# Kernel optimization log

Measured on AMD Instinct MI355X. Metric: run time of the kernel, lower is better.

## Reference

```python
import jax, jax.numpy as jnp
import numpy as np

M = 4096   # out_features
N = 4096   # in_features
K_NNZ = 204  # nnz per row -> keep_ratio ~ 0.05
T = 8192   # tokens (batch*seq)


def setup_inputs() -> dict:
    key = jax.random.key(0)
    k1, k2, k3, k4 = jax.random.split(key, 4)
    # CSR structure: K_NNZ unique sorted columns per row (constant index buffers)
    rng = np.random.default_rng(0)
    cols = np.argsort(rng.random((M, N)), axis=1)[:, :K_NNZ]
    cols = np.sort(cols, axis=1).astype(np.int32)
    col_idx = jnp.asarray(cols.reshape(-1))                      # [nnz]
    row_ids = jnp.asarray(np.repeat(np.arange(M, dtype=np.int32), K_NNZ))  # [nnz]
    x = jax.random.normal(k1, (T, N), dtype=jnp.float32)
    dense_weight = jax.random.normal(k2, (M, N), dtype=jnp.float32) * 0.02
    bias = jax.random.normal(k3, (M,), dtype=jnp.float32) * 0.02
    sparse_values = jax.random.normal(k4, (M * K_NNZ,), dtype=jnp.float32) * 0.02
    return {"x": x, "dense_weight": dense_weight, "bias": bias,
            "sparse_values": sparse_values, "row_ids": row_ids, "col_idx": col_idx}


def reference(x, dense_weight, bias, sparse_values, row_ids, col_idx):
    # sp_add: scatter CSR values into the frozen dense weight (W = W_dense + W_sparse)
    W = dense_weight.at[row_ids, col_idx].add(sparse_values)     # [M, N]
    # sp_mm hot path: y = x @ W^T + b
    return jnp.dot(x, W.T) + bias                                # [T, M]
```

## Files before the change

### kernel.cpp

```cpp
#include <hip/hip_runtime.h>


typedef __attribute__((ext_vector_type(8))) __bf16 bf16x8;
typedef __attribute__((ext_vector_type(4))) float f32x4;
typedef __attribute__((ext_vector_type(8))) unsigned short u16x8;

#define BARRIER()   asm volatile("s_barrier" ::: "memory")
#define WAITVM0()   asm volatile("s_waitcnt vmcnt(0)" ::: "memory")

__device__ __forceinline__ unsigned short f2bf(float f) {
  unsigned int u = __builtin_bit_cast(unsigned int, f);
  u += 0x7FFFu + ((u >> 16) & 1u);
  return (unsigned short)(u >> 16);
}

__global__ __launch_bounds__(256) void cvt_f32_bf16(
    const float* __restrict__ s, unsigned short* __restrict__ d, long n8) {
  long i = (long)blockIdx.x * blockDim.x + threadIdx.x;
  const long stride = (long)gridDim.x * blockDim.x;
  for (; i < n8; i += stride) {
    const float4* sp = (const float4*)(s + i * 8);
    float4 a = sp[0];
    float4 b = sp[1];
    u16x8 o;
    o[0] = f2bf(a.x); o[1] = f2bf(a.y); o[2] = f2bf(a.z); o[3] = f2bf(a.w);
    o[4] = f2bf(b.x); o[5] = f2bf(b.y); o[6] = f2bf(b.z); o[7] = f2bf(b.w);
    *(u16x8*)(d + i * 8) = o;
  }
}

__global__ __launch_bounds__(256) void sparse_scatter(
    const float* __restrict__ dense, const float* __restrict__ vals,
    const int* __restrict__ rows, const int* __restrict__ cols,
    unsigned short* __restrict__ Wb, int nnz, int K) {
  int i = blockIdx.x * blockDim.x + threadIdx.x;
  if (i < nnz) {
    size_t off = (size_t)rows[i] * (size_t)K + (size_t)cols[i];
    Wb[off] = f2bf(dense[off] + vals[i]);
  }
}

__global__ __launch_bounds__(512, 2) void gemm256p(
    const unsigned short* __restrict__ A,
    const unsigned short* __restrict__ B,
    const float* __restrict__ bias,
    float* __restrict__ C,
    int Tm, int Mn, int K) {
  extern __shared__ __align__(16) char smem[];

  const int tid  = threadIdx.x;
  const int lane = tid & 63;
  const int wid  = tid >> 6;
  const int wm = (wid >> 2) * 128;
  const int wn = (wid & 3) * 64;

  const int nwg = gridDim.x;
  int bid = blockIdx.x;
  if ((nwg & 7) == 0) bid = (bid & 7) * (nwg >> 3) + (bid >> 3);
  const int ntn = Mn >> 8;
  const int bm0 = (bid / ntn) << 8;
  const int bn0 = (bid % ntn) << 8;

  const int NT = K >> 6;

  const int sr  = tid >> 3;
  const int gq8 = ((tid & 7) ^ (sr & 7)) * 8;
  const unsigned short* Asrc = A + (size_t)(bm0 + sr) * K + gq8;
  const unsigned short* Bsrc = B + (size_t)(bn0 + sr) * K + gq8;
  const size_t r64 = (size_t)64 * K;
  const int ldst = tid * 16;

#define STAGEH(SRC, H, LDSB, KOFF) do {                                          \
    __builtin_amdgcn_global_load_lds(                                            \
      (const __attribute__((address_space(1))) void*)((SRC) + (size_t)(H)*2*r64 + (KOFF)), \
      (__attribute__((address_space(3))) void*)(smem + (LDSB) + ldst), 16, 0, 0);\
    __builtin_amdgcn_global_load_lds(                                            \
      (const __attribute__((address_space(1))) void*)((SRC) + (size_t)(H)*2*r64 + r64 + (KOFF)), \
      (__attribute__((address_space(3))) void*)(smem + (LDSB) + 8192 + ldst), 16, 0, 0); \
  } while (0)

  const int fr = lane & 15, cq = lane >> 4;
  const int f7 = fr & 7;
  const int q0 = ((cq ^ f7) << 4);
  const int q1 = (((4 + cq) ^ f7) << 4);
  const int arow = (wm + fr) * 128;
  const int brow = (wn + fr) * 128;

  f32x4 acc[8][4] = {};
  bf16x8 aq0[4], aq1[4], bA0[2], bA1[2], bB0[2], bB1[2];

  STAGEH(Asrc, 0, 0, 0);
  STAGEH(Asrc, 1, 16384, 0);
  STAGEH(Bsrc, 0, 32768, 0);
  STAGEH(Bsrc, 1, 49152, 0);
  WAITVM0();
  BARRIER();

#pragma unroll 2
  for (int t = 0; t < NT; ++t) {
    const char* Ab = smem + (t & 1) * 65536;
    const char* Bb = Ab + 32768;
    const int nbase = ((t & 1) ^ 1) * 65536;
    const int kn = (t + 1) * 64;
    const bool st = (t + 1 < NT);

#pragma unroll
    for (int m = 0; m < 4; ++m) {
      aq0[m] = *(const bf16x8*)(Ab + arow + m * 2048 + q0);
      aq1[m] = *(const bf16x8*)(Ab + arow + m * 2048 + q1);
    }
#pragma unroll
    for (int n = 0; n < 2; ++n) {
      bA0[n] = *(const bf16x8*)(Bb + brow + n * 2048 + q0);
      bA1[n] = *(const bf16x8*)(Bb + brow + n * 2048 + q1);
    }
    if (st) { STAGEH(Asrc, 0, nbase, kn); STAGEH(Asrc, 1, nbase + 16384, kn); }
    BARRIER();
    __builtin_amdgcn_s_setprio(1);
#pragma unroll
    for (int m = 0; m < 4; ++m)
#pragma unroll
      for (int n = 0; n < 2; ++n) {
        acc[m][n] = __builtin_amdgcn_mfma_f32_16x16x32_bf16(aq0[m], bA0[n], acc[m][n], 0, 0, 0);
        acc[m][n] = __builtin_amdgcn_mfma_f32_16x16x32_bf16(aq1[m], bA1[n], acc[m][n], 0, 0, 0);
      }
    __builtin_amdgcn_s_setprio(0);
    BARRIER();

#pragma unroll
    for (int n = 0; n < 2; ++n) {
      bB0[n] = *(const bf16x8*)(Bb + brow + (n + 2) * 2048 + q0);
      bB1[n] = *(const bf16x8*)(Bb + brow + (n + 2) * 2048 + q1);
    }
    if (st) { STAGEH(Bsrc, 0, nbase + 32768, kn); STAGEH(Bsrc, 1, nbase + 49152, kn); }
    BARRIER();
    __builtin_amdgcn_s_setprio(1);
#pragma unroll
    for (int m = 0; m < 4; ++m)
#pragma unroll
      for (int n = 0; n < 2; ++n) {
        acc[m][n + 2] = __builtin_amdgcn_mfma_f32_16x16x32_bf16(aq0[m], bB0[n], acc[m][n + 2], 0, 0, 0);
        acc[m][n + 2] = __builtin_amdgcn_mfma_f32_16x16x32_bf16(aq1[m], bB1[n], acc[m][n + 2], 0, 0, 0);
      }
    __builtin_amdgcn_s_setprio(0);
    BARRIER();

#pragma unroll
    for (int m = 0; m < 4; ++m) {
      aq0[m] = *(const bf16x8*)(Ab + arow + (m + 4) * 2048 + q0);
      aq1[m] = *(const bf16x8*)(Ab + arow + (m + 4) * 2048 + q1);
    }
    BARRIER();
    __builtin_amdgcn_s_setprio(1);
#pragma unroll
    for (int m = 0; m < 4; ++m)
#pragma unroll
      for (int n = 0; n < 2; ++n) {
        acc[m + 4][n] = __builtin_amdgcn_mfma_f32_16x16x32_bf16(aq0[m], bA0[n], acc[m + 4][n], 0, 0, 0);
        acc[m + 4][n] = __builtin_amdgcn_mfma_f32_16x16x32_bf16(aq1[m], bA1[n], acc[m + 4][n], 0, 0, 0);
      }
    __builtin_amdgcn_s_setprio(0);
    BARRIER();

    __builtin_amdgcn_s_setprio(1);
#pragma unroll
    for (int m = 0; m < 4; ++m)
#pragma unroll
      for (int n = 0; n < 2; ++n) {
        acc[m + 4][n + 2] = __builtin_amdgcn_mfma_f32_16x16x32_bf16(aq0[m], bB0[n], acc[m + 4][n + 2], 0, 0, 0);
        acc[m + 4][n + 2] = __builtin_amdgcn_mfma_f32_16x16x32_bf16(aq1[m], bB1[n], acc[m + 4][n + 2], 0, 0, 0);
      }
    __builtin_amdgcn_s_setprio(0);
    WAITVM0();
    BARRIER();
  }
#undef STAGEH

  const int c4 = cq * 4;
#pragma unroll
  for (int n = 0; n < 4; ++n) {
    const int col = bn0 + wn + n * 16 + fr;
    const float bv = bias[col];
#pragma unroll
    for (int m = 0; m < 8; ++m) {
      const size_t rowb = (size_t)(bm0 + wm + m * 16 + c4);
#pragma unroll
      for (int q = 0; q < 4; ++q)
        C[(rowb + q) * (size_t)Mn + col] = acc[m][n][q] + bv;
    }
  }
}

extern "C" void kernel_launch(void* const* d_in, const int* in_sizes, int n_in,
                              void* d_out, int out_size, void* d_ws, size_t ws_size,
                              hipStream_t stream) {
  const float* x     = (const float*)d_in[0];
  const float* dw    = (const float*)d_in[1];
  const float* bias  = (const float*)d_in[2];
  const float* sv    = (const float*)d_in[3];
  const int*   rows  = (const int*)d_in[4];
  const int*   cols  = (const int*)d_in[5];
  float* out = (float*)d_out;

  const int  Mn = in_sizes[2];
  const long wElems = (long)in_sizes[1];
  const int  K  = (int)(wElems / Mn);
  const long xElems = (long)in_sizes[0];
  const int  Tm = (int)(xElems / K);
  const int  nnz = in_sizes[3];

  unsigned short* Wb = (unsigned short*)d_ws;
  unsigned short* Xb = Wb + wElems;

  cvt_f32_bf16<<<2048, 256, 0, stream>>>(dw, Wb, wElems / 8);
  sparse_scatter<<<(nnz + 255) / 256, 256, 0, stream>>>(dw, sv, rows, cols, Wb, nnz, K);
  cvt_f32_bf16<<<2048, 256, 0, stream>>>(x, Xb, xElems / 8);

  dim3 grid((Tm >> 8) * (Mn >> 8));
  gemm256p<<<grid, 512, 131072, stream>>>(Xb, Wb, bias, out, Tm, Mn, K);
}
```

Baseline: 313.6 us.

## Restructure GEMM main loop into 8-phase ping-pong with staggered partial vmcnt waits

Unrolls the K loop by two with fixed even/odd LDS buffers and spreads the global-to-LDS stages across eight MFMA phases. B tiles are prefetched one step further ahead, so each iteration waits with vmcnt(4) instead of draining all outstanding loads. It also adds lgkmcnt waits and scheduling barriers before each MFMA quad. The goal is to overlap memory latency with compute. The trade-off is more complex buffer-hazard reasoning and some risk of races, since loads are issued into buffers still being read.

Measured after the change: 306.7 us. 1.02x faster.

```diff
diff --git a/kernel.cpp b/kernel.cpp
--- a/kernel.cpp
+++ b/kernel.cpp
@@ -6,7 +6,9 @@
 typedef __attribute__((ext_vector_type(8))) unsigned short u16x8;
 
 #define BARRIER()   asm volatile("s_barrier" ::: "memory")
-#define WAITVM0()   asm volatile("s_waitcnt vmcnt(0)" ::: "memory")
+#define WAITLGKM0() asm volatile("s_waitcnt lgkmcnt(0)" ::: "memory")
+#define WAITVM(n)   asm volatile("s_waitcnt vmcnt(" #n ")" ::: "memory")
+#define SCHED0()    __builtin_amdgcn_sched_barrier(0)
 
 __device__ __forceinline__ unsigned short f2bf(float f) {
   unsigned int u = __builtin_bit_cast(unsigned int, f);
@@ -40,7 +42,7 @@
   }
 }
 
-__global__ __launch_bounds__(512, 2) void gemm256p(
+__global__ __launch_bounds__(512, 2) void gemm8p(
     const unsigned short* __restrict__ A,
     const unsigned short* __restrict__ B,
     const float* __restrict__ bias,
@@ -93,87 +95,112 @@
   STAGEH(Asrc, 1, 16384, 0);
   STAGEH(Bsrc, 0, 32768, 0);
   STAGEH(Bsrc, 1, 49152, 0);
-  WAITVM0();
+  STAGEH(Bsrc, 0, 98304, 64);
+  STAGEH(Bsrc, 1, 114688, 64);
+  WAITVM(4);
   BARRIER();
 
-#pragma unroll 2
-  for (int t = 0; t < NT; ++t) {
-    const char* Ab = smem + (t & 1) * 65536;
-    const char* Bb = Ab + 32768;
-    const int nbase = ((t & 1) ^ 1) * 65536;
-    const int kn = (t + 1) * 64;
-    const bool st = (t + 1 < NT);
-
-#pragma unroll
-    for (int m = 0; m < 4; ++m) {
-      aq0[m] = *(const bf16x8*)(Ab + arow + m * 2048 + q0);
-      aq1[m] = *(const bf16x8*)(Ab + arow + m * 2048 + q1);
-    }
-#pragma unroll
-    for (int n = 0; n < 2; ++n) {
-      bA0[n] = *(const bf16x8*)(Bb + brow + n * 2048 + q0);
-      bA1[n] = *(const bf16x8*)(Bb + brow + n * 2048 + q1);
-    }
-    if (st) { STAGEH(Asrc, 0, nbase, kn); STAGEH(Asrc, 1, nbase + 16384, kn); }
-    BARRIER();
-    __builtin_amdgcn_s_setprio(1);
-#pragma unroll
-    for (int m = 0; m < 4; ++m)
-#pragma unroll
-      for (int n = 0; n < 2; ++n) {
-        acc[m][n] = __builtin_amdgcn_mfma_f32_16x16x32_bf16(aq0[m], bA0[n], acc[m][n], 0, 0, 0);
-        acc[m][n] = __builtin_amdgcn_mfma_f32_16x16x32_bf16(aq1[m], bA1[n], acc[m][n], 0, 0, 0);
-      }
-    __builtin_amdgcn_s_setprio(0);
-    BARRIER();
-
-#pragma unroll
-    for (int n = 0; n < 2; ++n) {
-      bB0[n] = *(const bf16x8*)(Bb + brow + (n + 2) * 2048 + q0);
-      bB1[n] = *(const bf16x8*)(Bb + brow + (n + 2) * 2048 + q1);
-    }
-    if (st) { STAGEH(Bsrc, 0, nbase + 32768, kn); STAGEH(Bsrc, 1, nbase + 49152, kn); }
-    BARRIER();
-    __builtin_amdgcn_s_setprio(1);
-#pragma unroll
-    for (int m = 0; m < 4; ++m)
-#pragma unroll
-      for (int n = 0; n < 2; ++n) {
-        acc[m][n + 2] = __builtin_amdgcn_mfma_f32_16x16x32_bf16(aq0[m], bB0[n], acc[m][n + 2], 0, 0, 0);
-        acc[m][n + 2] = __builtin_amdgcn_mfma_f32_16x16x32_bf16(aq1[m], bB1[n], acc[m][n + 2], 0, 0, 0);
-      }
-    __builtin_amdgcn_s_setprio(0);
-    BARRIER();
-
-#pragma unroll
-    for (int m = 0; m < 4; ++m) {
-      aq0[m] = *(const bf16x8*)(Ab + arow + (m + 4) * 2048 + q0);
-      aq1[m] = *(const bf16x8*)(Ab + arow + (m + 4) * 2048 + q1);
-    }
-    BARRIER();
-    __builtin_amdgcn_s_setprio(1);
-#pragma unroll
-    for (int m = 0; m < 4; ++m)
-#pragma unroll
-      for (int n = 0; n < 2; ++n) {
-        acc[m + 4][n] = __builtin_amdgcn_mfma_f32_16x16x32_bf16(aq0[m], bA0[n], acc[m + 4][n], 0, 0, 0);
-        acc[m + 4][n] = __builtin_amdgcn_mfma_f32_16x16x32_bf16(aq1[m], bA1[n], acc[m + 4][n], 0, 0, 0);
-      }
-    __builtin_amdgcn_s_setprio(0);
-    BARRIER();
-
-    __builtin_amdgcn_s_setprio(1);
-#pragma unroll
-    for (int m = 0; m < 4; ++m)
-#pragma unroll
-      for (int n = 0; n < 2; ++n) {
-        acc[m + 4][n + 2] = __builtin_amdgcn_mfma_f32_16x16x32_bf16(aq0[m], bB0[n], acc[m + 4][n + 2], 0, 0, 0);
-        acc[m + 4][n + 2] = __builtin_amdgcn_mfma_f32_16x16x32_bf16(aq1[m], bB1[n], acc[m + 4][n + 2], 0, 0, 0);
-      }
-    __builtin_amdgcn_s_setprio(0);
-    WAITVM0();
-    BARRIER();
-  }
+#define QUAD(MB, NB, AQ0, AQ1, BL0, BL1) do {                                    \
+    __builtin_amdgcn_s_setprio(1);                                               \
+    _Pragma("unroll")                                                            \
+    for (int m = 0; m < 4; ++m)                                                  \
+      _Pragma("unroll")                                                          \
+      for (int n = 0; n < 2; ++n) {                                              \
+        acc[m+(MB)][n+(NB)] = __builtin_amdgcn_mfma_f32_16x16x32_bf16(           \
+            AQ0[m], BL0[n], acc[m+(MB)][n+(NB)], 0, 0, 0);                       \
+        acc[m+(MB)][n+(NB)] = __builtin_amdgcn_mfma_f32_16x16x32_bf16(           \
+            AQ1[m], BL1[n], acc[m+(MB)][n+(NB)], 0, 0, 0);                       \
+      }                                                                          \
+    __builtin_amdgcn_s_setprio(0);                                               \
+  } while (0)
+
+  for (int j = 0; j < (NT >> 1); ++j) {
+    const int t2 = 2 * j + 2, t3 = 2 * j + 3;
+    const int k1 = (2 * j + 1) << 6, k2 = t2 << 6, k3 = t3 << 6;
+    const char* AbE = smem;            const char* BbE = smem + 32768;
+    const char* AbO = smem + 65536;    const char* BbO = smem + 98304;
+
+#pragma unroll
+    for (int m = 0; m < 4; ++m) {
+      aq0[m] = *(const bf16x8*)(AbE + arow + m * 2048 + q0);
+      aq1[m] = *(const bf16x8*)(AbE + arow + m * 2048 + q1);
+    }
+#pragma unroll
+    for (int n = 0; n < 2; ++n) {
+      bA0[n] = *(const bf16x8*)(BbE + brow + n * 2048 + q0);
+      bA1[n] = *(const bf16x8*)(BbE + brow + n * 2048 + q1);
+    }
+    STAGEH(Asrc, 0, 65536, k1);
+    BARRIER(); WAITLGKM0(); SCHED0();
+    QUAD(0, 0, aq0, aq1, bA0, bA1);
+    BARRIER();
+
+#pragma unroll
+    for (int n = 0; n < 2; ++n) {
+      bB0[n] = *(const bf16x8*)(BbE + brow + (n + 2) * 2048 + q0);
+      bB1[n] = *(const bf16x8*)(BbE + brow + (n + 2) * 2048 + q1);
+    }
+    STAGEH(Asrc, 1, 81920, k1);
+    BARRIER(); WAITLGKM0(); SCHED0();
+    QUAD(0, 2, aq0, aq1, bB0, bB1);
+    BARRIER();
+
+#pragma unroll
+    for (int m = 0; m < 4; ++m) {
+      aq0[m] = *(const bf16x8*)(AbE + arow + (m + 4) * 2048 + q0);
+      aq1[m] = *(const bf16x8*)(AbE + arow + (m + 4) * 2048 + q1);
+    }
+    if (t2 < NT) STAGEH(Bsrc, 0, 32768, k2);
+    BARRIER(); WAITLGKM0(); SCHED0();
+    QUAD(4, 0, aq0, aq1, bA0, bA1);
+    BARRIER();
+
+    if (t2 < NT) STAGEH(Bsrc, 1, 49152, k2);
+    QUAD(4, 2, aq0, aq1, bB0, bB1);
+    if (t2 < NT) { WAITVM(4); } else { WAITVM(0); }
+    BARRIER();
+
+#pragma unroll
+    for (int m = 0; m < 4; ++m) {
+      aq0[m] = *(const bf16x8*)(AbO + arow + m * 2048 + q0);
+      aq1[m] = *(const bf16x8*)(AbO + arow + m * 2048 + q1);
+    }
+#pragma unroll
+    for (int n = 0; n < 2; ++n) {
+      bA0[n] = *(const bf16x8*)(BbO + brow + n * 2048 + q0);
+      bA1[n] = *(const bf16x8*)(BbO + brow + n * 2048 + q1);
+    }
+    if (t2 < NT) STAGEH(Asrc, 0, 0, k2);
+    BARRIER(); WAITLGKM0(); SCHED0();
+    QUAD(0, 0, aq0, aq1, bA0, bA1);
+    BARRIER();
+
+#pragma unroll
+    for (int n = 0; n < 2; ++n) {
+      bB0[n] = *(const bf16x8*)(BbO + brow + (n + 2) * 2048 + q0);
+      bB1[n] = *(const bf16x8*)(BbO + brow + (n + 2) * 2048 + q1);
+    }
+    if (t2 < NT) STAGEH(Asrc, 1, 16384, k2);
+    BARRIER(); WAITLGKM0(); SCHED0();
+    QUAD(0, 2, aq0, aq1, bB0, bB1);
+    BARRIER();
+
+#pragma unroll
+    for (int m = 0; m < 4; ++m) {
+      aq0[m] = *(const bf16x8*)(AbO + arow + (m + 4) * 2048 + q0);
+      aq1[m] = *(const bf16x8*)(AbO + arow + (m + 4) * 2048 + q1);
+    }
+    if (t3 < NT) STAGEH(Bsrc, 0, 98304, k3);
+    BARRIER(); WAITLGKM0(); SCHED0();
+    QUAD(4, 0, aq0, aq1, bA0, bA1);
+    BARRIER();
+
+    if (t3 < NT) STAGEH(Bsrc, 1, 114688, k3);
+    QUAD(4, 2, aq0, aq1, bB0, bB1);
+    if (t3 < NT) { WAITVM(4); } else if (t2 < NT) { WAITVM(0); }
+    BARRIER();
+  }
+#undef QUAD
 #undef STAGEH
 
   const int c4 = cq * 4;
@@ -217,5 +244,5 @@
   cvt_f32_bf16<<<2048, 256, 0, stream>>>(x, Xb, xElems / 8);
 
   dim3 grid((Tm >> 8) * (Mn >> 8));
-  gemm256p<<<grid, 512, 131072, stream>>>(Xb, Wb, bias, out, Tm, Mn, K);
-}
+  gemm8p<<<grid, 512, 131072, stream>>>(Xb, Wb, bias, out, Tm, Mn, K);
+}
```
